# Kernel optimization log

Hardware: AMD Instinct MI355X
Metric: run time of the kernel (lower is better)

## Reference

```python
import jax, jax.numpy as jnp
import numpy as np

START_AGE = 0
END_AGE = 100
LAMBDA_1 = 0.2
LAMBDA_2 = 0.05
EPS = 1e-3

N = 524288
WIDTH = END_AGE + 1 - START_AGE  # 101


def setup_inputs() -> dict:
    key = jax.random.key(0)
    k1, k2 = jax.random.split(key)
    inp = jax.random.normal(k1, (N, WIDTH), dtype=jnp.float32)
    target = jax.random.randint(k2, (N,), 0, WIDTH, dtype=jnp.int32)
    return {"input": inp, "target": target}


def reference(input, target):
    # softmax over age bins
    p = jax.nn.softmax(input, axis=1)                                  # [N, W]
    a = jnp.arange(START_AGE, END_AGE + 1, dtype=jnp.float32)          # [W]
    tf = target.astype(jnp.float32)
    # expected age per sample
    mean = jnp.sum(p * a, axis=1)                                      # [N]
    mean_loss = jnp.mean((mean - tf) ** 2) / 2.0
    # vectorized one-hot gather: prob of ground-truth bin
    prob_gt = jnp.take_along_axis(p, target[:, None].astype(jnp.int32), axis=1)  # [N,1]
    # mask of bins with prob strictly below the GT prob; detached in the original
    mask = jax.lax.stop_gradient((p < prob_gt).astype(p.dtype))        # [N, W]
    p_not_K = mask * p
    residue_loss = jnp.mean(jnp.sum(-(p_not_K + EPS) * jnp.log(p_not_K + EPS), axis=1))
    batch_average_K = jnp.sum(mask == 0).astype(jnp.float32) / N
    return (LAMBDA_1 * mean_loss, LAMBDA_2 * residue_loss, batch_average_K)
```

## Files before the change

kernel.cpp:

```cpp
#include <hip/hip_runtime.h>

#define N_ROWS   524288
#define W_BINS   101
#define EPS_F    1e-3f
#define NTHREADS 256
#define NBLK     (N_ROWS / NTHREADS)
#define NWAVES   (N_ROWS / 64)

__global__ __launch_bounds__(256, 3) void mrl_main(const float* __restrict__ x,
                                                   const int* __restrict__ tgt,
                                                   float4* __restrict__ partial) {
    const int row = blockIdx.x * NTHREADS + threadIdx.x;
    const float* __restrict__ r = x + (size_t)row * W_BINS;

    const int   t  = tgt[row];
    const float xt = r[t];

    float e[W_BINS];
    float se0 = 0.f, se1 = 0.f, sa0 = 0.f, sa1 = 0.f;
    #pragma unroll
    for (int i = 0; i < 100; i += 2) {
        float v0 = r[i];
        float v1 = r[i + 1];
        float E0 = __expf(v0);
        float E1 = __expf(v1);
        e[i] = E0;     e[i + 1] = E1;
        se0 += E0;     sa0 += E0 * (float)i;
        se1 += E1;     sa1 += E1 * (float)(i + 1);
    }
    {
        float E = __expf(r[100]);
        e[100] = E;
        se0 += E; sa0 += E * 100.0f;
    }
    const float se  = se0 + se1;
    const float sea = sa0 + sa1;

    const float egt = __expf(xt);
    const float inv = __builtin_amdgcn_rcpf(se);
    const float d   = sea * inv - (float)t;
    float sq = d * d;

    float rc0 = 0.f, rc1 = 0.f;
    int   kk  = 0;
    #pragma unroll
    for (int i = 0; i < 100; i += 2) {
        bool  l0 = e[i]     < egt;
        bool  l1 = e[i + 1] < egt;
        float q0 = (l0 ? e[i]     * inv : 0.f) + EPS_F;
        float q1 = (l1 ? e[i + 1] * inv : 0.f) + EPS_F;
        rc0 -= q0 * __logf(q0);
        rc1 -= q1 * __logf(q1);
        kk  += (l0 ? 0 : 1) + (l1 ? 0 : 1);
    }
    {
        bool  l = e[100] < egt;
        float q = (l ? e[100] * inv : 0.f) + EPS_F;
        rc0 -= q * __logf(q);
        kk  += l ? 0 : 1;
    }
    float rc = rc0 + rc1;
    float kf = (float)kk;

    #pragma unroll
    for (int off = 32; off >= 1; off >>= 1) {
        sq += __shfl_xor(sq, off);
        rc += __shfl_xor(rc, off);
        kf += __shfl_xor(kf, off);
    }
    if ((threadIdx.x & 63) == 0) {
        partial[row >> 6] = make_float4(sq, rc, kf, 0.0f);
    }
}

__global__ __launch_bounds__(256) void mrl_reduce(const float4* __restrict__ partial,
                                                  float* __restrict__ out) {
    double s = 0.0, r = 0.0, k = 0.0;
    for (int i = threadIdx.x; i < NWAVES; i += 256) {
        float4 v = partial[i];
        s += (double)v.x; r += (double)v.y; k += (double)v.z;
    }
    #pragma unroll
    for (int off = 32; off >= 1; off >>= 1) {
        s += __shfl_xor(s, off);
        r += __shfl_xor(r, off);
        k += __shfl_xor(k, off);
    }
    __shared__ double sd[12];
    const int w = threadIdx.x >> 6;
    if ((threadIdx.x & 63) == 0) { sd[w * 3 + 0] = s; sd[w * 3 + 1] = r; sd[w * 3 + 2] = k; }
    __syncthreads();
    if (threadIdx.x == 0) {
        double S = sd[0] + sd[3] + sd[6] + sd[9];
        double R = sd[1] + sd[4] + sd[7] + sd[10];
        double K = sd[2] + sd[5] + sd[8] + sd[11];
        const double n = (double)N_ROWS;
        out[0] = (float)(0.1  * (S / n));
        out[1] = (float)(0.05 * (R / n));
        out[2] = (float)(K / n);
    }
}

extern "C" void kernel_launch(void* const* d_in, const int* in_sizes, int n_in,
                              void* d_out, int out_size, void* d_ws, size_t ws_size,
                              hipStream_t stream) {
    const float* x   = (const float*)d_in[0];
    const int*   tgt = (const int*)d_in[1];
    float*  out     = (float*)d_out;
    float4* partial = (float4*)d_ws;

    mrl_main<<<NBLK, NTHREADS, 0, stream>>>(x, tgt, partial);
    mrl_reduce<<<1, 256, 0, stream>>>(partial, out);
}
```

Baseline: 322.9 us.

## Stage row tiles in LDS with coalesced float4 loads, one wave per block

Each 64-thread block now cooperatively copies a contiguous 64-row tile into shared memory using coalesced float4 loads, then each lane processes its row from LDS. This replaces strided per-thread global reads of 101-float rows. The odd row stride avoids LDS bank conflicts. The large per-block LDS footprint limits resident waves per CU, and load and compute are not overlapped.

```diff
diff --git a/kernel.cpp b/kernel.cpp
--- a/kernel.cpp
+++ b/kernel.cpp
@@ -3,40 +3,53 @@
 #define N_ROWS   524288
 #define W_BINS   101
 #define EPS_F    1e-3f
-#define NTHREADS 256
-#define NBLK     (N_ROWS / NTHREADS)
-#define NWAVES   (N_ROWS / 64)
+#define RPB      64
+#define NBLK     (N_ROWS / RPB)
+#define TILE_F   (RPB * W_BINS)
+#define TILE_V4  (TILE_F / 4)
 
-__global__ __launch_bounds__(256, 3) void mrl_main(const float* __restrict__ x,
-                                                   const int* __restrict__ tgt,
-                                                   float4* __restrict__ partial) {
-    const int row = blockIdx.x * NTHREADS + threadIdx.x;
-    const float* __restrict__ r = x + (size_t)row * W_BINS;
+__global__ __launch_bounds__(64) void mrl_main(const float* __restrict__ x,
+                                               const int* __restrict__ tgt,
+                                               float4* __restrict__ partial) {
+    __shared__ float sm[TILE_F];
+    const int lane = threadIdx.x;
 
-    const int   t  = tgt[row];
-    const float xt = r[t];
+    const float4* __restrict__ g  = (const float4*)(x + (size_t)blockIdx.x * TILE_F);
+    float4* __restrict__       s4 = (float4*)sm;
+
+    #pragma unroll
+    for (int q = 0; q < 25; ++q) {
+        s4[q * 64 + lane] = g[q * 64 + lane];
+    }
+    if (lane < 16) {
+        s4[1600 + lane] = g[1600 + lane];
+    }
+
+    const int t = tgt[blockIdx.x * RPB + lane];
+
+    __syncthreads();
+
+    const int rb = lane * W_BINS;
 
     float e[W_BINS];
     float se0 = 0.f, se1 = 0.f, sa0 = 0.f, sa1 = 0.f;
     #pragma unroll
     for (int i = 0; i < 100; i += 2) {
-        float v0 = r[i];
-        float v1 = r[i + 1];
-        float E0 = __expf(v0);
-        float E1 = __expf(v1);
+        float E0 = __expf(sm[rb + i]);
+        float E1 = __expf(sm[rb + i + 1]);
         e[i] = E0;     e[i + 1] = E1;
         se0 += E0;     sa0 += E0 * (float)i;
         se1 += E1;     sa1 += E1 * (float)(i + 1);
     }
     {
-        float E = __expf(r[100]);
+        float E = __expf(sm[rb + 100]);
         e[100] = E;
         se0 += E; sa0 += E * 100.0f;
     }
     const float se  = se0 + se1;
     const float sea = sa0 + sa1;
 
-    const float egt = __expf(xt);
+    const float egt = __expf(sm[rb + t]);
     const float inv = __builtin_amdgcn_rcpf(se);
     const float d   = sea * inv - (float)t;
     float sq = d * d;
@@ -68,15 +81,15 @@
         rc += __shfl_xor(rc, off);
         kf += __shfl_xor(kf, off);
     }
-    if ((threadIdx.x & 63) == 0) {
-        partial[row >> 6] = make_float4(sq, rc, kf, 0.0f);
+    if (lane == 0) {
+        partial[blockIdx.x] = make_float4(sq, rc, kf, 0.0f);
     }
 }
 
 __global__ __launch_bounds__(256) void mrl_reduce(const float4* __restrict__ partial,
                                                   float* __restrict__ out) {
     double s = 0.0, r = 0.0, k = 0.0;
-    for (int i = threadIdx.x; i < NWAVES; i += 256) {
+    for (int i = threadIdx.x; i < NBLK; i += 256) {
         float4 v = partial[i];
         s += (double)v.x; r += (double)v.y; k += (double)v.z;
     }
@@ -109,6 +122,6 @@
     float*  out     = (float*)d_out;
     float4* partial = (float4*)d_ws;
 
-    mrl_main<<<NBLK, NTHREADS, 0, stream>>>(x, tgt, partial);
+    mrl_main<<<NBLK, RPB, 0, stream>>>(x, tgt, partial);
     mrl_reduce<<<1, 256, 0, stream>>>(partial, out);
 }
```

New measurement: 307.0 us. 1.05x faster.
